# Kernel tuning notes

Hardware: AMD Instinct MI355X
Metric: run time of the kernel (lower is better)

## Reference

```python
import jax, jax.numpy as jnp
import numpy as np

INPUT_DIM = 256
OUTPUT_DIM = 256
GRID_SIZE = 32


def setup_inputs() -> dict:
    key = jax.random.key(0)
    k1, k2 = jax.random.split(key)
    x = jax.random.normal(k1, (4096, INPUT_DIM), dtype=jnp.float32)
    # fouriercoeffs: randn(2, out, in, grid) / (sqrt(in) * sqrt(grid))  (smooth_initialization=False)
    scale = np.sqrt(INPUT_DIM) * np.sqrt(GRID_SIZE)
    fouriercoeffs = jax.random.normal(k2, (2, OUTPUT_DIM, INPUT_DIM, GRID_SIZE), dtype=jnp.float32) / scale
    bias = jnp.zeros((1, OUTPUT_DIM), dtype=jnp.float32)
    return {"x": x, "fouriercoeffs": fouriercoeffs, "bias": bias}


def reference(x, fouriercoeffs, bias):
    # x: [N, input_dim]; fouriercoeffs: [2, out, in, grid]; bias: [1, out]
    grid_size = fouriercoeffs.shape[-1]
    k = jnp.arange(1, grid_size + 1, dtype=x.dtype)  # [grid]
    phase = x[:, :, None] * k  # [N, in, grid]
    c = jnp.cos(phase)
    s = jnp.sin(phase)
    # contraction over (in, grid) -> GEMM-like einsum; same math as the
    # original broadcast-multiply-sum but without the [N,out,in,grid] blowup
    y = jnp.einsum("big,jig->bj", c, fouriercoeffs[0])
    y = y + jnp.einsum("big,jig->bj", s, fouriercoeffs[1])
    y = y + bias
    return y
```

## Files before the change

kernel.cpp:

```cpp
#include <hip/hip_runtime.h>
#include <hip/hip_bf16.h>
#include <cstdint>

typedef __attribute__((ext_vector_type(8))) short  short8;
typedef __attribute__((ext_vector_type(4))) float  f32x4;
typedef __attribute__((ext_vector_type(4))) unsigned uint4v;

#define N_ROWS   4096
#define IN_DIM   256
#define OUT_DIM  256
#define GRIDSZ   32
#define K_TOTAL  16384
#define SPLITK   8
#define KCHUNK   2048
#define BM       128
#define BK       64
#define STEPS    32

__global__ void convert_coeffs(const float* __restrict__ w,
                               __hip_bfloat16* __restrict__ bm) {
    int gid = blockIdx.x * 256 + threadIdx.x;
    int j = gid >> 14;
    int k = gid & (K_TOTAL - 1);
    int i = k >> 6;
    int r = k & 63;
    int g = r >> 1;
    int p = r & 1;
    float v = w[(((p << 8) + j) * 256 + i) * 32 + g];
    bm[gid] = __float2bfloat16(v);
}

__global__ void bias_fill(const float* __restrict__ bias, float* __restrict__ out) {
    int gid = blockIdx.x * 256 + threadIdx.x;
    out[gid] = bias[gid & (OUT_DIM - 1)];
}

__device__ __forceinline__ void gld_lds16(const void* g, void* l) {
    __builtin_amdgcn_global_load_lds(
        (const __attribute__((address_space(1))) void*)(uintptr_t)g,
        (__attribute__((address_space(3))) void*)(uintptr_t)l, 16, 0, 0);
}

__device__ __forceinline__ unsigned f2bf(float f) {
    unsigned u = __builtin_bit_cast(unsigned, f);
    return (u + 0x7fffu + ((u >> 16) & 1u)) >> 16;
}

__global__ __launch_bounds__(512, 2) void fkan_gemm(const float* __restrict__ x,
                                                    const __hip_bfloat16* __restrict__ bm,
                                                    float* __restrict__ out) {
    __shared__ float  x_lds[STEPS][BM];
    __shared__ short  A_lds[2][BM * BK];
    __shared__ short  B_lds[2][OUT_DIM * BK];

    const int tid  = threadIdx.x;
    const int lane = tid & 63;
    const int wid  = tid >> 6;
    const int wm   = wid >> 2;
    const int wn   = wid & 3;

    const int bid = blockIdx.x;
    const int ks  = bid & 7;
    const int mb  = bid >> 3;
    const int m0  = mb * BM;
    const int i0  = ks * STEPS;
    const int kbase = ks * KCHUNK;

    #pragma unroll
    for (int s2 = 0; s2 < 2; ++s2) {
        int slot = tid + s2 * 512;
        int m  = slot >> 3;
        int c4 = slot & 7;
        f32x4 xv = *(const f32x4*)&x[(m0 + m) * IN_DIM + i0 + c4 * 4];
        #pragma unroll
        for (int q = 0; q < 4; ++q) x_lds[c4 * 4 + q][m] = xv[q];
    }
    __syncthreads();

    f32x4 acc[4][4];
    #pragma unroll
    for (int a = 0; a < 4; ++a)
        #pragma unroll
        for (int b = 0; b < 4; ++b) acc[a][b] = (f32x4){0.f, 0.f, 0.f, 0.f};

    const int am = tid & 127;
    const int ah = tid >> 7;

    auto stage_B = [&](int s, int buf) {
        int kg = kbase + s * BK;
        #pragma unroll
        for (int r = 0; r < 4; ++r) {
            int jl = wid * 32 + r * 8 + (lane >> 3);
            int cg = (lane & 7) ^ (jl & 7);
            const __hip_bfloat16* src = bm + jl * K_TOTAL + kg + cg * 8;
            gld_lds16(src, &B_lds[buf][(wid * 32 + r * 8) * BK]);
        }
    };

    auto gen_A = [&](int s, int buf) {
        float xv = x_lds[s][am];
        float c1, s1; __sincosf(xv, &s1, &c1);
        float cg, sg; __sincosf((float)(8 * ah + 1) * xv, &sg, &cg);
        unsigned pk[8];
        #pragma unroll
        for (int e = 0; e < 8; ++e) {
            pk[e] = f2bf(cg) | (f2bf(sg) << 16);
            float cn = cg * c1 - sg * s1;
            sg = sg * c1 + cg * s1;
            cg = cn;
        }
        int base = am * BK;
        uint4v w0 = {pk[0], pk[1], pk[2], pk[3]};
        uint4v w1 = {pk[4], pk[5], pk[6], pk[7]};
        *(uint4v*)&A_lds[buf][base + (((2 * ah    ) ^ (am & 7)) << 3)] = w0;
        *(uint4v*)&A_lds[buf][base + (((2 * ah + 1) ^ (am & 7)) << 3)] = w1;
    };

    auto compute = [&](int buf) {
        const int rA = lane & 15;
        const int cA = lane >> 4;
        #pragma unroll
        for (int kf = 0; kf < 2; ++kf) {
            short8 af[4], bf[4];
            #pragma unroll
            for (int mf = 0; mf < 4; ++mf) {
                int row = wm * 64 + mf * 16 + rA;
                int ch  = (kf * 4 + cA) ^ (rA & 7);
                af[mf] = *(const short8*)&A_lds[buf][row * BK + ch * 8];
            }
            #pragma unroll
            for (int nf = 0; nf < 4; ++nf) {
                int row = wn * 64 + nf * 16 + rA;
                int ch  = (kf * 4 + cA) ^ (rA & 7);
                bf[nf] = *(const short8*)&B_lds[buf][row * BK + ch * 8];
            }
            #pragma unroll
            for (int mf = 0; mf < 4; ++mf)
                #pragma unroll
                for (int nf = 0; nf < 4; ++nf)
                    acc[mf][nf] = __builtin_amdgcn_mfma_f32_16x16x32_bf16(
                        af[mf], bf[nf], acc[mf][nf], 0, 0, 0);
        }
    };

    stage_B(0, 0);
    gen_A(0, 0);
    int cur = 0;
    for (int s = 0; s < STEPS; ++s) {
        __syncthreads();
        if (s + 1 < STEPS) { stage_B(s + 1, cur ^ 1); gen_A(s + 1, cur ^ 1); }
        compute(cur);
        cur ^= 1;
    }

    const int cl = lane & 15;
    const int rl = (lane >> 4) * 4;
    #pragma unroll
    for (int mf = 0; mf < 4; ++mf) {
        #pragma unroll
        for (int nf = 0; nf < 4; ++nf) {
            int row = m0 + wm * 64 + mf * 16 + rl;
            int col = wn * 64 + nf * 16 + cl;
            #pragma unroll
            for (int r2 = 0; r2 < 4; ++r2)
                atomicAdd(&out[(row + r2) * OUT_DIM + col], acc[mf][nf][r2]);
        }
    }
}

extern "C" void kernel_launch(void* const* d_in, const int* in_sizes, int n_in,
                              void* d_out, int out_size, void* d_ws, size_t ws_size,
                              hipStream_t stream) {
    const float* x      = (const float*)d_in[0];
    const float* coeffs = (const float*)d_in[1];
    const float* bias   = (const float*)d_in[2];
    float* out = (float*)d_out;
    __hip_bfloat16* bmat = (__hip_bfloat16*)d_ws;

    convert_coeffs<<<(OUT_DIM * K_TOTAL) / 256, 256, 0, stream>>>(coeffs, bmat);
    bias_fill<<<(N_ROWS * OUT_DIM) / 256, 256, 0, stream>>>(bias, out);
    fkan_gemm<<<SPLITK * (N_ROWS / BM), 512, 0, stream>>>(x, bmat, out);
}
```

Measured before the change: 139.9 us.

## Split output columns into two N tiles with 256-thread blocks and single-buffered A

```diff
diff --git a/kernel.cpp b/kernel.cpp
--- a/kernel.cpp
+++ b/kernel.cpp
@@ -9,11 +9,11 @@
 #define N_ROWS   4096
 #define IN_DIM   256
 #define OUT_DIM  256
-#define GRIDSZ   32
 #define K_TOTAL  16384
 #define SPLITK   8
 #define KCHUNK   2048
 #define BM       128
+#define BN       128
 #define BK       64
 #define STEPS    32
 
@@ -46,45 +46,28 @@
     return (u + 0x7fffu + ((u >> 16) & 1u)) >> 16;
 }
 
-__global__ __launch_bounds__(512, 2) void fkan_gemm(const float* __restrict__ x,
+__global__ __launch_bounds__(256, 2) void fkan_gemm(const float* __restrict__ x,
                                                     const __hip_bfloat16* __restrict__ bm,
                                                     float* __restrict__ out) {
     __shared__ float  x_lds[STEPS][BM];
-    __shared__ short  A_lds[2][BM * BK];
-    __shared__ short  B_lds[2][OUT_DIM * BK];
+    __shared__ short  A_lds[BM * BK];
+    __shared__ short  B_lds[2][BN * BK];
 
     const int tid  = threadIdx.x;
     const int lane = tid & 63;
     const int wid  = tid >> 6;
-    const int wm   = wid >> 2;
-    const int wn   = wid & 3;
+    const int wm   = wid >> 1;
+    const int wn   = wid & 1;
 
     const int bid = blockIdx.x;
     const int ks  = bid & 7;
-    const int mb  = bid >> 3;
+    const int tt  = bid >> 3;
+    const int mb  = tt >> 1;
+    const int nb  = tt & 1;
     const int m0  = mb * BM;
+    const int n0  = nb * BN;
     const int i0  = ks * STEPS;
     const int kbase = ks * KCHUNK;
-
-    #pragma unroll
-    for (int s2 = 0; s2 < 2; ++s2) {
-        int slot = tid + s2 * 512;
-        int m  = slot >> 3;
-        int c4 = slot & 7;
-        f32x4 xv = *(const f32x4*)&x[(m0 + m) * IN_DIM + i0 + c4 * 4];
-        #pragma unroll
-        for (int q = 0; q < 4; ++q) x_lds[c4 * 4 + q][m] = xv[q];
-    }
-    __syncthreads();
-
-    f32x4 acc[4][4];
-    #pragma unroll
-    for (int a = 0; a < 4; ++a)
-        #pragma unroll
-        for (int b = 0; b < 4; ++b) acc[a][b] = (f32x4){0.f, 0.f, 0.f, 0.f};
-
-    const int am = tid & 127;
-    const int ah = tid >> 7;
 
     auto stage_B = [&](int s, int buf) {
         int kg = kbase + s * BK;
@@ -92,29 +75,39 @@
         for (int r = 0; r < 4; ++r) {
             int jl = wid * 32 + r * 8 + (lane >> 3);
             int cg = (lane & 7) ^ (jl & 7);
-            const __hip_bfloat16* src = bm + jl * K_TOTAL + kg + cg * 8;
+            const __hip_bfloat16* src = bm + (size_t)(n0 + jl) * K_TOTAL + kg + cg * 8;
             gld_lds16(src, &B_lds[buf][(wid * 32 + r * 8) * BK]);
         }
     };
 
-    auto gen_A = [&](int s, int buf) {
+    const int am = tid & 127;
+    const int ah = tid >> 7;
+
+    auto gen_A = [&](int s) {
         float xv = x_lds[s][am];
         float c1, s1; __sincosf(xv, &s1, &c1);
-        float cg, sg; __sincosf((float)(8 * ah + 1) * xv, &sg, &cg);
-        unsigned pk[8];
+        float cg, sg; __sincosf((float)(16 * ah + 1) * xv, &sg, &cg);
+        unsigned pk[16];
         #pragma unroll
-        for (int e = 0; e < 8; ++e) {
+        for (int e = 0; e < 16; ++e) {
             pk[e] = f2bf(cg) | (f2bf(sg) << 16);
             float cn = cg * c1 - sg * s1;
             sg = sg * c1 + cg * s1;
             cg = cn;
         }
         int base = am * BK;
-        uint4v w0 = {pk[0], pk[1], pk[2], pk[3]};
-        uint4v w1 = {pk[4], pk[5], pk[6], pk[7]};
-        *(uint4v*)&A_lds[buf][base + (((2 * ah    ) ^ (am & 7)) << 3)] = w0;
-        *(uint4v*)&A_lds[buf][base + (((2 * ah + 1) ^ (am & 7)) << 3)] = w1;
+        #pragma unroll
+        for (int q = 0; q < 4; ++q) {
+            uint4v w = {pk[4 * q], pk[4 * q + 1], pk[4 * q + 2], pk[4 * q + 3]};
+            *(uint4v*)&A_lds[base + (((4 * ah + q) ^ (am & 7)) << 3)] = w;
+        }
     };
+
+    f32x4 acc[4][4];
+    #pragma unroll
+    for (int a = 0; a < 4; ++a)
+        #pragma unroll
+        for (int b = 0; b < 4; ++b) acc[a][b] = (f32x4){0.f, 0.f, 0.f, 0.f};
 
     auto compute = [&](int buf) {
         const int rA = lane & 15;
@@ -126,7 +119,7 @@
             for (int mf = 0; mf < 4; ++mf) {
                 int row = wm * 64 + mf * 16 + rA;
                 int ch  = (kf * 4 + cA) ^ (rA & 7);
-                af[mf] = *(const short8*)&A_lds[buf][row * BK + ch * 8];
+                af[mf] = *(const short8*)&A_lds[row * BK + ch * 8];
             }
             #pragma unroll
             for (int nf = 0; nf < 4; ++nf) {
@@ -144,12 +137,25 @@
     };
 
     stage_B(0, 0);
-    gen_A(0, 0);
+    #pragma unroll
+    for (int s2 = 0; s2 < 4; ++s2) {
+        int slot = tid + s2 * 256;
+        int m  = slot >> 3;
+        int c4 = slot & 7;
+        f32x4 xv = *(const f32x4*)&x[(size_t)(m0 + m) * IN_DIM + i0 + c4 * 4];
+        #pragma unroll
+        for (int q = 0; q < 4; ++q) x_lds[c4 * 4 + q][m] = xv[q];
+    }
+    __syncthreads();
+    gen_A(0);
+
     int cur = 0;
     for (int s = 0; s < STEPS; ++s) {
         __syncthreads();
-        if (s + 1 < STEPS) { stage_B(s + 1, cur ^ 1); gen_A(s + 1, cur ^ 1); }
+        if (s + 1 < STEPS) stage_B(s + 1, cur ^ 1);
         compute(cur);
+        __syncthreads();
+        if (s + 1 < STEPS) gen_A(s + 1);
         cur ^= 1;
     }
 
@@ -160,10 +166,10 @@
         #pragma unroll
         for (int nf = 0; nf < 4; ++nf) {
             int row = m0 + wm * 64 + mf * 16 + rl;
-            int col = wn * 64 + nf * 16 + cl;
+            int col = n0 + wn * 64 + nf * 16 + cl;
             #pragma unroll
             for (int r2 = 0; r2 < 4; ++r2)
-                atomicAdd(&out[(row + r2) * OUT_DIM + col], acc[mf][nf][r2]);
+                atomicAdd(&out[(size_t)(row + r2) * OUT_DIM + col], acc[mf][nf][r2]);
         }
     }
 }
@@ -179,5 +185,5 @@
 
     convert_coeffs<<<(OUT_DIM * K_TOTAL) / 256, 256, 0, stream>>>(coeffs, bmat);
     bias_fill<<<(N_ROWS * OUT_DIM) / 256, 256, 0, stream>>>(bias, out);
-    fkan_gemm<<<SPLITK * (N_ROWS / BM), 512, 0, stream>>>(x, bmat, out);
+    fkan_gemm<<<SPLITK * (N_ROWS / BM) * (OUT_DIM / BN), 256, 0, stream>>>(x, bmat, out);
 }
```

Measured after the change: 144.0 us. 2.9% more time.
